# Kernel tuning notes

Measured on AMD Instinct MI355X. Metric: run time of the kernel, lower is better.

The kernel has to match this reference:

```python
import jax, jax.numpy as jnp
import numpy as np

EPS = 1e-12  # matches torch F.normalize clamp_min eps
SCALE = 20.0
NEG = -1e9


def l2norm(x):
    return x / jnp.maximum(jnp.linalg.norm(x, axis=-1, keepdims=True), EPS)


def setup_inputs() -> dict:
    key = jax.random.key(0)
    B, P, A, DV, DT, E = 32, 192, 30, 768, 768, 256
    ks = jax.random.split(key, 8)
    visual_feature = jax.random.normal(ks[0], (B, 1 + P, DV), jnp.float32)
    textual_feature = jax.random.normal(ks[1], (B, 1 + A, DT), jnp.float32)
    att_nums = jax.random.randint(ks[2], (B,), 1, A + 1)  # valid attr counts >=1
    # mask==1 marks padded attribute slots (consistent with att_nums)
    mask = (jnp.arange(A)[None, :] >= att_nums[:, None]).astype(jnp.int32)
    W_vis = 0.02 * jax.random.normal(ks[3], (E, DV), jnp.float32)
    W_txt = 0.02 * jax.random.normal(ks[4], (E, DT), jnp.float32)
    W_patch = 0.02 * jax.random.normal(ks[5], (E, DV), jnp.float32)
    W_att = 0.02 * jax.random.normal(ks[6], (E, DT), jnp.float32)
    z = jnp.zeros((E,), jnp.float32)
    return {
        "visual_feature": visual_feature, "textual_feature": textual_feature,
        "mask": mask, "att_nums": att_nums,
        "W_vis": W_vis, "b_vis": z, "W_txt": W_txt, "b_txt": z,
        "W_patch": W_patch, "b_patch": z, "W_att": W_att, "b_att": z,
    }


def reference(visual_feature, textual_feature, mask, att_nums,
              W_vis, b_vis, W_txt, b_txt, W_patch, b_patch, W_att, b_att):
    # token splits + linear projections
    visual_embed = visual_feature[:, 0] @ W_vis.T + b_vis        # [Bv, E]
    patch = visual_feature[:, 1:] @ W_patch.T + b_patch           # [Bv, P, E]
    textual_embed = textual_feature[:, 0] @ W_txt.T + b_txt       # [Bt, E]
    att = textual_feature[:, 1:] @ W_att.T + b_att                # [Bt, A, E]

    pad = mask.astype(bool)                                       # [Bt, A], True = padded

    # attention 1: each text's attributes attend over every image's patches
    s1 = jax.nn.relu(jnp.einsum('tae,vpe->vtap', l2norm(att), l2norm(patch))) * SCALE
    attn1 = jax.nn.softmax(s1, axis=-1)                           # [Bv, Bt, A, P]
    attend_patch = jnp.einsum('vtap,vpe->vtae', attn1, patch)     # [Bv, Bt, A, E]
    attend_patch = jnp.where(pad[None, :, :, None], 0.0, attend_patch)

    # attention 2: each image's patches attend over every text's attributes (masked)
    s2 = jax.nn.relu(jnp.einsum('vpe,tae->tvpa', l2norm(patch), l2norm(att))) * SCALE
    s2 = jnp.where(pad[:, None, None, :], NEG, s2)                # [Bt, Bv, P, A]
    attn2 = jax.nn.softmax(s2, axis=-1)
    attend_att = jnp.einsum('tvpa,tae->tvpe', attn2, att)         # [Bt, Bv, P, E]

    # local similarity
    ap = l2norm(attend_patch)                                     # [Bv, Bt, A, E]
    aa = l2norm(attend_att)                                       # [Bt, Bv, P, E]
    an = att_nums.astype(aa.dtype)
    sim = jnp.einsum('tvpe,vtae->tvpa', aa, ap) / an[:, None, None, None]
    local_similarity = sim.sum(axis=2).mean(axis=2)               # [Bt, Bv]

    # training-path global embeds
    patch_mean = patch.mean(axis=1)                               # [Bv, E]
    att_mean = (att / an[:, None, None]).sum(axis=1)              # [Bt, E]

    return (visual_embed, textual_embed, patch_mean, att_mean, local_similarity)
```

## Files before the change

### kernel.cpp

```cpp
#include <hip/hip_runtime.h>
#include <math.h>

#define D_IN 768
#define E_DIM 256
#define NB 32
#define NP 192
#define NA 30

#define A_SLOTS (452 * 24 * 64)
#define B_SLOTS (4 * 16 * 24 * 64)

typedef __attribute__((ext_vector_type(8))) __bf16 bf16x8;
typedef __attribute__((ext_vector_type(4))) float f32x4;

__device__ __forceinline__ bf16x8 cvt8(float4 a, float4 b) {
    bf16x8 v;
    v[0]=(__bf16)a.x; v[1]=(__bf16)a.y; v[2]=(__bf16)a.z; v[3]=(__bf16)a.w;
    v[4]=(__bf16)b.x; v[5]=(__bf16)b.y; v[6]=(__bf16)b.z; v[7]=(__bf16)b.w;
    return v;
}

__global__ __launch_bounds__(256) void prepack_kernel(
    const float* __restrict__ vf, const float* __restrict__ tf,
    const float* __restrict__ Wp, const float* __restrict__ Wa,
    const float* __restrict__ Wv, const float* __restrict__ Wt,
    __bf16* __restrict__ Apack, __bf16* __restrict__ Bpack,
    float* __restrict__ out_zero)
{
    const int s = blockIdx.x * 256 + threadIdx.x;
    if (s < 16384) out_zero[s] = 0.f;
    if (s < A_SLOTS) {
        const int r16 = s / 1536;
        const int rem = s - r16 * 1536;
        const int kt = rem >> 6, l = rem & 63;
        const int row16 = l & 15;
        const int k0 = kt * 32 + (l >> 4) * 8;
        const float* src;
        if (r16 < 384) {
            const int v = r16 / 12, sub = r16 - 12 * v;
            src = vf + (size_t)(v * 193 + 1 + sub * 16 + row16) * D_IN;
        } else if (r16 < 448) {
            const int u = r16 - 384, t = u >> 1, half = u & 1;
            const int ridx = half * 16 + row16;
            const int r = (ridx < NA) ? ridx : 0;
            src = tf + (size_t)(t * 31 + 1 + r) * D_IN;
        } else if (r16 < 450) {
            src = vf + (size_t)((r16 - 448) * 16 + row16) * 193 * D_IN;
        } else {
            src = tf + (size_t)((r16 - 450) * 16 + row16) * 31 * D_IN;
        }
        float4 f0 = *(const float4*)&src[k0];
        float4 f1 = *(const float4*)&src[k0 + 4];
        *(bf16x8*)&Apack[(size_t)s * 8] = cvt8(f0, f1);
    } else {
        const int u = s - A_SLOTS;
        const int mat = u / 24576;
        const int rem = u - mat * 24576;
        const int ntile = rem / 1536;
        const int rem2 = rem - ntile * 1536;
        const int kt = rem2 >> 6, l = rem2 & 63;
        const float* W;
        if (mat == 0)      W = Wp;
        else if (mat == 1) W = Wa;
        else if (mat == 2) W = Wv;
        else               W = Wt;
        const int k0 = kt * 32 + (l >> 4) * 8;
        const float* src = W + (size_t)(ntile * 16 + (l & 15)) * D_IN;
        float4 f0 = *(const float4*)&src[k0];
        float4 f1 = *(const float4*)&src[k0 + 4];
        *(bf16x8*)&Bpack[(size_t)u * 8] = cvt8(f0, f1);
    }
}

__global__ __launch_bounds__(256) void gemm_pack_kernel(
    const __bf16* __restrict__ Apack, const __bf16* __restrict__ Bpack,
    const float* __restrict__ bv, const float* __restrict__ bt,
    const float* __restrict__ bp, const float* __restrict__ ba,
    const int* __restrict__ att_nums,
    float* __restrict__ out_vis, float* __restrict__ out_txt,
    float* __restrict__ out_pm, float* __restrict__ out_am,
    __bf16* __restrict__ pn_frag, __bf16* __restrict__ pB_frag,
    __bf16* __restrict__ an_frag, __bf16* __restrict__ attT_frag)
{
    __shared__ float LDSf[16 * 260];
    __shared__ float invn_s[16];

    const int r16 = blockIdx.x;
    const int tid = threadIdx.x;
    const int w = tid >> 6, l = tid & 63, q = l >> 4, n15 = l & 15;
    const int mat = (r16 < 384) ? 0 : (r16 < 448) ? 1 : (r16 < 450) ? 2 : 3;
    const float* bias = (mat == 0) ? bp : (mat == 1) ? ba : (mat == 2) ? bv : bt;

    const __bf16* Ab = Apack + (size_t)r16 * 24 * 512 + l * 8;
    const __bf16* Bb = Bpack + ((size_t)(mat * 16 + w * 4) * 24 * 512) + l * 8;

    f32x4 acc[4];
    #pragma unroll
    for (int n = 0; n < 4; ++n) { f32x4 z = {0.f,0.f,0.f,0.f}; acc[n] = z; }

    #pragma unroll 6
    for (int kt = 0; kt < 24; ++kt) {
        bf16x8 a = *(const bf16x8*)&Ab[kt * 512];
        #pragma unroll
        for (int nt = 0; nt < 4; ++nt) {
            bf16x8 b = *(const bf16x8*)&Bb[(size_t)nt * 24 * 512 + kt * 512];
            acc[nt] = __builtin_amdgcn_mfma_f32_16x16x32_bf16(a, b, acc[nt], 0, 0, 0);
        }
    }

    #pragma unroll
    for (int nt = 0; nt < 4; ++nt) {
        const int col = w * 64 + nt * 16 + n15;
        const float b = bias[col];
        #pragma unroll
        for (int r = 0; r < 4; ++r)
            LDSf[(q * 4 + r) * 260 + col] = acc[nt][r] + b;
    }
    __syncthreads();

    if (mat >= 2) {
        float* outp = (mat == 2) ? out_vis : out_txt;
        const int rowbase = (mat == 2) ? (r16 - 448) * 16 : (r16 - 450) * 16;
        #pragma unroll
        for (int i = 0; i < 16; ++i)
            outp[(rowbase + i) * E_DIM + tid] = LDSf[i * 260 + tid];
        return;
    }

    const bool is_patch = (mat == 0);
    int vc = 0, mt = 0, t = 0, Av = 1;
    if (is_patch) {
        const int v = r16 / 12, sub = r16 - 12 * v;
        vc = v * 6 + (sub >> 1);  mt = sub & 1;
    } else {
        const int u = r16 - 384;
        t = u >> 1;  mt = u & 1;  Av = att_nums[t];
    }

    {
        const int row = tid >> 4, seg = tid & 15;
        const float* rr = &LDSf[row * 260 + seg * 16];
        float ssq = 0.f;
        #pragma unroll
        for (int j = 0; j < 16; ++j) ssq += rr[j] * rr[j];
        ssq += __shfl_xor(ssq, 1, 64);
        ssq += __shfl_xor(ssq, 2, 64);
        ssq += __shfl_xor(ssq, 4, 64);
        ssq += __shfl_xor(ssq, 8, 64);
        if (seg == 0) {
            const bool valid = is_patch || (mt * 16 + row < NA);
            invn_s[row] = valid ? 1.f / fmaxf(sqrtf(ssq), 1e-12f) : 0.f;
        }
    }
    {
        const int nrows = is_patch ? 16 : (mt == 0 ? 16 : 14);
        float s = 0.f;
        for (int r = 0; r < nrows; ++r) s += LDSf[r * 260 + tid];
        if (is_patch) atomicAdd(&out_pm[(r16 / 12) * E_DIM + tid], s * (1.f / 192.f));
        else          atomicAdd(&out_am[t * E_DIM + tid], s / (float)Av);
    }
    __syncthreads();

    {
        __bf16* dstn = (is_patch ? pn_frag + (size_t)vc * 8192
                                 : an_frag + (size_t)t * 8192) + (size_t)mt * 4096;
        #pragma unroll
        for (int ii = 0; ii < 2; ++ii) {
            const int s2 = tid + 256 * ii;
            const int koct = s2 >> 6, lane = s2 & 63;
            const int rloc = lane & 15;
            const int e0 = koct * 32 + (lane >> 4) * 8;
            const float inr = invn_s[rloc];
            const float* src = &LDSf[rloc * 260 + e0];
            bf16x8 vv;
            #pragma unroll
            for (int j = 0; j < 8; ++j) vv[j] = (__bf16)(src[j] * inr);
            *(bf16x8*)&dstn[(size_t)s2 * 8] = vv;
        }
    }
    {
        __bf16* dstb = is_patch ? pB_frag + (size_t)vc * 8192
                                : attT_frag + (size_t)t * 8192;
        #pragma unroll
        for (int ii = 0; ii < 2; ++ii) {
            const int s2 = tid + 256 * ii;
            const int nt = s2 >> 5, li = s2 & 31;
            const int lane = 32 * mt + li;
            const int p0 = (li >> 4) * 8;
            const int e = nt * 16 + (li & 15);
            bf16x8 vv;
            #pragma unroll
            for (int j = 0; j < 8; ++j) {
                float val = LDSf[(p0 + j) * 260 + e];
                if (!is_patch && (mt * 16 + p0 + j >= NA)) val = 0.f;
                vv[j] = (__bf16)val;
            }
            *(bf16x8*)&dstb[(size_t)(nt * 64 + lane) * 8] = vv;
        }
    }
}

__global__ __launch_bounds__(256, 3) void pair_mfma_kernel(
    const __bf16* __restrict__ pn_frag, const __bf16* __restrict__ pB_frag,
    const __bf16* __restrict__ an_frag, const __bf16* __restrict__ attT_frag,
    const int* __restrict__ att_nums, float* __restrict__ out_sim)
{
    __shared__ __align__(16) __bf16 an_s[8192];
    __shared__ __align__(16) __bf16 Xa_s[1024];
    __shared__ __align__(16) __bf16 XaT_s[1024];
    __shared__ float red_s[128];
    __shared__ float wred_s[4];

    const int v = blockIdx.x, t = blockIdx.y;
    const int tid = threadIdx.x;
    const int w = tid >> 6, l = tid & 63, q = l >> 4, n15 = l & 15;
    const int Av = att_nums[t];
    const int mt = w >> 1, at = w & 1;

    {
        const __bf16* s1 = an_frag + (size_t)t * 8192;
        #pragma unroll
        for (int i = 0; i < 4; ++i) {
            const int slot = tid + 256 * i;
            *(bf16x8*)&an_s[slot * 8] = *(const bf16x8*)&s1[slot * 8];
        }
    }
    __syncthreads();

    const __bf16* atb = attT_frag + (size_t)t * 8192;

    f32x4 apacc[2][4];
    #pragma unroll
    for (int m = 0; m < 2; ++m)
        #pragma unroll
        for (int n = 0; n < 4; ++n) { f32x4 z = {0.f,0.f,0.f,0.f}; apacc[m][n] = z; }
    float sa_acc[4] = {0.f, 0.f, 0.f, 0.f};

    for (int c = 0; c < 6; ++c) {
        const __bf16* pnb = pn_frag + (size_t)(v * 6 + c) * 8192;
        const __bf16* pbb = pB_frag + (size_t)(v * 6 + c) * 8192;

        bf16x8 pb[4], ab[4];
        #pragma unroll
        for (int n = 0; n < 4; ++n) {
            pb[n] = *(const bf16x8*)&pbb[((w * 4 + n) * 64 + l) * 8];
            ab[n] = *(const bf16x8*)&atb[((w * 4 + n) * 64 + l) * 8];
        }

        {
            f32x4 sacc = {0.f, 0.f, 0.f, 0.f};
            #pragma unroll
            for (int kp = 0; kp < 8; ++kp) {
                bf16x8 af  = *(const bf16x8*)&pnb[((mt * 8 + kp) * 64 + l) * 8];
                bf16x8 bf_ = *(const bf16x8*)&an_s[((at * 8 + kp) * 64 + l) * 8];
                sacc = __builtin_amdgcn_mfma_f32_16x16x32_bf16(af, bf_, sacc, 0, 0, 0);
            }
            const int a = at * 16 + n15;
            #pragma unroll
            for (int r = 0; r < 4; ++r) {
                const int pcl = q * 4 + r;
                const int pcc = mt * 16 + pcl;
                float xvv = (a < Av) ? __expf(fmaxf(20.f * sacc[r], 0.f)) : 0.f;
                __bf16 h = (__bf16)xvv;
                Xa_s[mt * 512 + (pcl + 16 * (a >> 3)) * 8 + (a & 7)] = h;
                XaT_s[at * 512 + (n15 + 16 * (pcc >> 3)) * 8 + (pcc & 7)] = h;
            }
        }
        __syncthreads();

        f32x4 aacc[2][4];
        {
            bf16x8 xa0 = *(const bf16x8*)&Xa_s[l * 8];
            bf16x8 xa1 = *(const bf16x8*)&Xa_s[512 + l * 8];
            bf16x8 xt0 = *(const bf16x8*)&XaT_s[l * 8];
            bf16x8 xt1 = *(const bf16x8*)&XaT_s[512 + l * 8];
            #pragma unroll
            for (int n = 0; n < 4; ++n) {
                f32x4 z = {0.f, 0.f, 0.f, 0.f};
                aacc[0][n] = __builtin_amdgcn_mfma_f32_16x16x32_bf16(xa0, ab[n], z, 0, 0, 0);
                aacc[1][n] = __builtin_amdgcn_mfma_f32_16x16x32_bf16(xa1, ab[n], z, 0, 0, 0);
                apacc[0][n] = __builtin_amdgcn_mfma_f32_16x16x32_bf16(xt0, pb[n], apacc[0][n], 0, 0, 0);
                apacc[1][n] = __builtin_amdgcn_mfma_f32_16x16x32_bf16(xt1, pb[n], apacc[1][n], 0, 0, 0);
            }
        }
        #pragma unroll
        for (int mt2 = 0; mt2 < 2; ++mt2)
            #pragma unroll
            for (int r = 0; r < 4; ++r) {
                float ssq = 0.f;
                #pragma unroll
                for (int n = 0; n < 4; ++n) { float vv = aacc[mt2][n][r]; ssq += vv * vv; }
                ssq += __shfl_xor(ssq, 1, 64);
                ssq += __shfl_xor(ssq, 2, 64);
                ssq += __shfl_xor(ssq, 4, 64);
                ssq += __shfl_xor(ssq, 8, 64);
                if (n15 == 0) red_s[(mt2 * 16 + q * 4 + r) * 4 + w] = ssq;
            }
        __syncthreads();
        #pragma unroll
        for (int mt2 = 0; mt2 < 2; ++mt2)
            #pragma unroll
            for (int r = 0; r < 4; ++r) {
                const int row = mt2 * 16 + q * 4 + r;
                const float s = red_s[row * 4] + red_s[row * 4 + 1]
                              + red_s[row * 4 + 2] + red_s[row * 4 + 3];
                const float inr = 1.f / fmaxf(sqrtf(s), 1e-12f);
                #pragma unroll
                for (int n = 0; n < 4; ++n) sa_acc[n] += aacc[mt2][n][r] * inr;
            }
    }

    __syncthreads();
    #pragma unroll
    for (int mt2 = 0; mt2 < 2; ++mt2)
        #pragma unroll
        for (int r = 0; r < 4; ++r) {
            float ssq = 0.f;
            #pragma unroll
            for (int n = 0; n < 4; ++n) { float vv = apacc[mt2][n][r]; ssq += vv * vv; }
            ssq += __shfl_xor(ssq, 1, 64);
            ssq += __shfl_xor(ssq, 2, 64);
            ssq += __shfl_xor(ssq, 4, 64);
            ssq += __shfl_xor(ssq, 8, 64);
            if (n15 == 0) red_s[(mt2 * 16 + q * 4 + r) * 4 + w] = ssq;
        }
    __syncthreads();

    float inr_ap[2][4];
    #pragma unroll
    for (int mt2 = 0; mt2 < 2; ++mt2)
        #pragma unroll
        for (int r = 0; r < 4; ++r) {
            const int row = mt2 * 16 + q * 4 + r;
            const float s = red_s[row * 4] + red_s[row * 4 + 1]
                          + red_s[row * 4 + 2] + red_s[row * 4 + 3];
            inr_ap[mt2][r] = 1.f / fmaxf(sqrtf(s), 1e-12f);
        }

    float prod = 0.f;
    #pragma unroll
    for (int n = 0; n < 4; ++n) {
        float sp = 0.f;
        #pragma unroll
        for (int mt2 = 0; mt2 < 2; ++mt2)
            #pragma unroll
            for (int r = 0; r < 4; ++r)
                sp += apacc[mt2][n][r] * inr_ap[mt2][r];
        float saf = sa_acc[n];
        saf += __shfl_xor(saf, 16, 64);
        saf += __shfl_xor(saf, 32, 64);
        float spf = sp;
        spf += __shfl_xor(spf, 16, 64);
        spf += __shfl_xor(spf, 32, 64);
        prod += saf * spf;
    }
    prod += __shfl_xor(prod, 1, 64);
    prod += __shfl_xor(prod, 2, 64);
    prod += __shfl_xor(prod, 4, 64);
    prod += __shfl_xor(prod, 8, 64);
    prod += __shfl_xor(prod, 16, 64);
    prod += __shfl_xor(prod, 32, 64);
    if (l == 0) wred_s[w] = prod;
    __syncthreads();
    if (tid == 0)
        out_sim[t * NB + v] = (wred_s[0] + wred_s[1] + wred_s[2] + wred_s[3]) * 0.25f
                              / ((float)Av * 30.f);
}

extern "C" void kernel_launch(void* const* d_in, const int* in_sizes, int n_in,
                              void* d_out, int out_size, void* d_ws, size_t ws_size,
                              hipStream_t stream)
{
    const float* vf = (const float*)d_in[0];
    const float* tf = (const float*)d_in[1];
    const int*   an = (const int*)d_in[3];
    const float* Wv = (const float*)d_in[4];
    const float* bv = (const float*)d_in[5];
    const float* Wt = (const float*)d_in[6];
    const float* bt = (const float*)d_in[7];
    const float* Wp = (const float*)d_in[8];
    const float* bp = (const float*)d_in[9];
    const float* Wa = (const float*)d_in[10];
    const float* ba = (const float*)d_in[11];

    float* out = (float*)d_out;
    float* out_vis = out;
    float* out_txt = out + 8192;
    float* out_pm  = out + 16384;
    float* out_am  = out + 24576;
    float* out_sim = out + 32768;

    __bf16* Apack = (__bf16*)d_ws;
    __bf16* Bpack = Apack + (size_t)A_SLOTS * 8;
    __bf16* frag0 = Bpack + (size_t)B_SLOTS * 8;
    __bf16* pn_frag   = frag0;
    __bf16* pB_frag   = frag0 + 1572864;
    __bf16* an_frag   = frag0 + 3145728;
    __bf16* attT_frag = frag0 + 3407872;

    prepack_kernel<<<(A_SLOTS + B_SLOTS) / 256, 256, 0, stream>>>(
        vf, tf, Wp, Wa, Wv, Wt, Apack, Bpack, out + 16384);

    gemm_pack_kernel<<<452, 256, 0, stream>>>(
        Apack, Bpack, bv, bt, bp, ba, an,
        out_vis, out_txt, out_pm, out_am,
        pn_frag, pB_frag, an_frag, attT_frag);

    pair_mfma_kernel<<<dim3(NB, NB), 256, 0, stream>>>(
        pn_frag, pB_frag, an_frag, attT_frag, an, out_sim);
}
```

Before: 149.6 us.

## Split GEMM K across 8 waves and restructure pair kernel to process chunk pairs

The projection GEMM kernel now runs 512 threads per block and splits the K dimension across two halves of waves, combining the partial sums through an extra LDS buffer. The pair kernel now processes two patch chunks per iteration. Each wave computes full-width attribute rows, so the attended-attribute norm is reduced in registers instead of through an LDS round trip, and there are half as many barriers. The cost is higher register pressure (16 accumulator tiles per wave) and an extra LDS reduction stage in the GEMM.

Result: slower. 178.4 us (+19.2%).

```diff
diff --git a/kernel.cpp b/kernel.cpp
--- a/kernel.cpp
+++ b/kernel.cpp
@@ -72,7 +72,7 @@
     }
 }
 
-__global__ __launch_bounds__(256) void gemm_pack_kernel(
+__global__ __launch_bounds__(512) void gemm_pack_kernel(
     const __bf16* __restrict__ Apack, const __bf16* __restrict__ Bpack,
     const float* __restrict__ bv, const float* __restrict__ bt,
     const float* __restrict__ bp, const float* __restrict__ ba,
@@ -83,23 +83,26 @@
     __bf16* __restrict__ an_frag, __bf16* __restrict__ attT_frag)
 {
     __shared__ float LDSf[16 * 260];
+    __shared__ float LDSp[16 * 260];
     __shared__ float invn_s[16];
 
     const int r16 = blockIdx.x;
     const int tid = threadIdx.x;
     const int w = tid >> 6, l = tid & 63, q = l >> 4, n15 = l & 15;
+    const int kh = w >> 2, wq = w & 3;
     const int mat = (r16 < 384) ? 0 : (r16 < 448) ? 1 : (r16 < 450) ? 2 : 3;
     const float* bias = (mat == 0) ? bp : (mat == 1) ? ba : (mat == 2) ? bv : bt;
 
-    const __bf16* Ab = Apack + (size_t)r16 * 24 * 512 + l * 8;
-    const __bf16* Bb = Bpack + ((size_t)(mat * 16 + w * 4) * 24 * 512) + l * 8;
+    const __bf16* Ab = Apack + (size_t)r16 * 24 * 512 + (size_t)kh * 12 * 512 + l * 8;
+    const __bf16* Bb = Bpack + ((size_t)(mat * 16 + wq * 4) * 24 * 512)
+                             + (size_t)kh * 12 * 512 + l * 8;
 
     f32x4 acc[4];
     #pragma unroll
     for (int n = 0; n < 4; ++n) { f32x4 z = {0.f,0.f,0.f,0.f}; acc[n] = z; }
 
     #pragma unroll 6
-    for (int kt = 0; kt < 24; ++kt) {
+    for (int kt = 0; kt < 12; ++kt) {
         bf16x8 a = *(const bf16x8*)&Ab[kt * 512];
         #pragma unroll
         for (int nt = 0; nt < 4; ++nt) {
@@ -108,22 +111,37 @@
         }
     }
 
-    #pragma unroll
-    for (int nt = 0; nt < 4; ++nt) {
-        const int col = w * 64 + nt * 16 + n15;
-        const float b = bias[col];
-        #pragma unroll
-        for (int r = 0; r < 4; ++r)
-            LDSf[(q * 4 + r) * 260 + col] = acc[nt][r] + b;
+    if (kh == 1) {
+        #pragma unroll
+        for (int nt = 0; nt < 4; ++nt) {
+            const int col = wq * 64 + nt * 16 + n15;
+            #pragma unroll
+            for (int r = 0; r < 4; ++r)
+                LDSp[(q * 4 + r) * 260 + col] = acc[nt][r];
+        }
+    }
+    __syncthreads();
+    if (kh == 0) {
+        #pragma unroll
+        for (int nt = 0; nt < 4; ++nt) {
+            const int col = wq * 64 + nt * 16 + n15;
+            const float b = bias[col];
+            #pragma unroll
+            for (int r = 0; r < 4; ++r) {
+                const int row = q * 4 + r;
+                LDSf[row * 260 + col] = acc[nt][r] + LDSp[row * 260 + col] + b;
+            }
+        }
     }
     __syncthreads();
 
     if (mat >= 2) {
         float* outp = (mat == 2) ? out_vis : out_txt;
         const int rowbase = (mat == 2) ? (r16 - 448) * 16 : (r16 - 450) * 16;
-        #pragma unroll
-        for (int i = 0; i < 16; ++i)
-            outp[(rowbase + i) * E_DIM + tid] = LDSf[i * 260 + tid];
+        const int col = tid & 255, rh = tid >> 8;
+        #pragma unroll
+        for (int i = 0; i < 8; ++i)
+            outp[(rowbase + rh * 8 + i) * E_DIM + col] = LDSf[(rh * 8 + i) * 260 + col];
         return;
     }
 
@@ -138,21 +156,22 @@
     }
 
     {
-        const int row = tid >> 4, seg = tid & 15;
-        const float* rr = &LDSf[row * 260 + seg * 16];
+        const int row = tid >> 5, seg = tid & 31;
+        const float* rr = &LDSf[row * 260 + seg * 8];
         float ssq = 0.f;
         #pragma unroll
-        for (int j = 0; j < 16; ++j) ssq += rr[j] * rr[j];
+        for (int j = 0; j < 8; ++j) ssq += rr[j] * rr[j];
         ssq += __shfl_xor(ssq, 1, 64);
         ssq += __shfl_xor(ssq, 2, 64);
         ssq += __shfl_xor(ssq, 4, 64);
         ssq += __shfl_xor(ssq, 8, 64);
+        ssq += __shfl_xor(ssq, 16, 64);
         if (seg == 0) {
             const bool valid = is_patch || (mt * 16 + row < NA);
             invn_s[row] = valid ? 1.f / fmaxf(sqrtf(ssq), 1e-12f) : 0.f;
         }
     }
-    {
+    if (tid < 256) {
         const int nrows = is_patch ? 16 : (mt == 0 ? 16 : 14);
         float s = 0.f;
         for (int r = 0; r < nrows; ++r) s += LDSf[r * 260 + tid];
@@ -164,39 +183,33 @@
     {
         __bf16* dstn = (is_patch ? pn_frag + (size_t)vc * 8192
                                  : an_frag + (size_t)t * 8192) + (size_t)mt * 4096;
-        #pragma unroll
-        for (int ii = 0; ii < 2; ++ii) {
-            const int s2 = tid + 256 * ii;
-            const int koct = s2 >> 6, lane = s2 & 63;
-            const int rloc = lane & 15;
-            const int e0 = koct * 32 + (lane >> 4) * 8;
-            const float inr = invn_s[rloc];
-            const float* src = &LDSf[rloc * 260 + e0];
-            bf16x8 vv;
-            #pragma unroll
-            for (int j = 0; j < 8; ++j) vv[j] = (__bf16)(src[j] * inr);
-            *(bf16x8*)&dstn[(size_t)s2 * 8] = vv;
-        }
+        const int s2 = tid;
+        const int koct = s2 >> 6, lane = s2 & 63;
+        const int rloc = lane & 15;
+        const int e0 = koct * 32 + (lane >> 4) * 8;
+        const float inr = invn_s[rloc];
+        const float* src = &LDSf[rloc * 260 + e0];
+        bf16x8 vv;
+        #pragma unroll
+        for (int j = 0; j < 8; ++j) vv[j] = (__bf16)(src[j] * inr);
+        *(bf16x8*)&dstn[(size_t)s2 * 8] = vv;
     }
     {
         __bf16* dstb = is_patch ? pB_frag + (size_t)vc * 8192
                                 : attT_frag + (size_t)t * 8192;
-        #pragma unroll
-        for (int ii = 0; ii < 2; ++ii) {
-            const int s2 = tid + 256 * ii;
-            const int nt = s2 >> 5, li = s2 & 31;
-            const int lane = 32 * mt + li;
-            const int p0 = (li >> 4) * 8;
-            const int e = nt * 16 + (li & 15);
-            bf16x8 vv;
-            #pragma unroll
-            for (int j = 0; j < 8; ++j) {
-                float val = LDSf[(p0 + j) * 260 + e];
-                if (!is_patch && (mt * 16 + p0 + j >= NA)) val = 0.f;
-                vv[j] = (__bf16)val;
-            }
-            *(bf16x8*)&dstb[(size_t)(nt * 64 + lane) * 8] = vv;
-        }
+        const int s2 = tid;
+        const int nt = s2 >> 5, li = s2 & 31;
+        const int lane = 32 * mt + li;
+        const int p0 = (li >> 4) * 8;
+        const int e = nt * 16 + (li & 15);
+        bf16x8 vv;
+        #pragma unroll
+        for (int j = 0; j < 8; ++j) {
+            float val = LDSf[(p0 + j) * 260 + e];
+            if (!is_patch && (mt * 16 + p0 + j >= NA)) val = 0.f;
+            vv[j] = (__bf16)val;
+        }
+        *(bf16x8*)&dstb[(size_t)(nt * 64 + lane) * 8] = vv;
     }
 }
 
@@ -206,9 +219,10 @@
     const int* __restrict__ att_nums, float* __restrict__ out_sim)
 {
     __shared__ __align__(16) __bf16 an_s[8192];
-    __shared__ __align__(16) __bf16 Xa_s[1024];
-    __shared__ __align__(16) __bf16 XaT_s[1024];
+    __shared__ __align__(16) __bf16 Xa_s[2][1024];
+    __shared__ __align__(16) __bf16 XaT_s[2][1024];
     __shared__ float red_s[128];
+    __shared__ float sp_s[256];
     __shared__ float wred_s[4];
 
     const int v = blockIdx.x, t = blockIdx.y;
@@ -216,6 +230,7 @@
     const int w = tid >> 6, l = tid & 63, q = l >> 4, n15 = l & 15;
     const int Av = att_nums[t];
     const int mt = w >> 1, at = w & 1;
+    const int cp = w >> 1, mtx = w & 1;
 
     {
         const __bf16* s1 = an_frag + (size_t)t * 8192;
@@ -234,20 +249,14 @@
     for (int m = 0; m < 2; ++m)
         #pragma unroll
         for (int n = 0; n < 4; ++n) { f32x4 z = {0.f,0.f,0.f,0.f}; apacc[m][n] = z; }
-    float sa_acc[4] = {0.f, 0.f, 0.f, 0.f};
-
-    for (int c = 0; c < 6; ++c) {
-        const __bf16* pnb = pn_frag + (size_t)(v * 6 + c) * 8192;
-        const __bf16* pbb = pB_frag + (size_t)(v * 6 + c) * 8192;
-
-        bf16x8 pb[4], ab[4];
-        #pragma unroll
-        for (int n = 0; n < 4; ++n) {
-            pb[n] = *(const bf16x8*)&pbb[((w * 4 + n) * 64 + l) * 8];
-            ab[n] = *(const bf16x8*)&atb[((w * 4 + n) * 64 + l) * 8];
-        }
-
-        {
+    float sa_acc[16];
+    #pragma unroll
+    for (int n = 0; n < 16; ++n) sa_acc[n] = 0.f;
+
+    for (int i = 0; i < 3; ++i) {
+        #pragma unroll
+        for (int cc = 0; cc < 2; ++cc) {
+            const __bf16* pnb = pn_frag + (size_t)(v * 6 + 2 * i + cc) * 8192;
             f32x4 sacc = {0.f, 0.f, 0.f, 0.f};
             #pragma unroll
             for (int kp = 0; kp < 8; ++kp) {
@@ -262,108 +271,106 @@
                 const int pcc = mt * 16 + pcl;
                 float xvv = (a < Av) ? __expf(fmaxf(20.f * sacc[r], 0.f)) : 0.f;
                 __bf16 h = (__bf16)xvv;
-                Xa_s[mt * 512 + (pcl + 16 * (a >> 3)) * 8 + (a & 7)] = h;
-                XaT_s[at * 512 + (n15 + 16 * (pcc >> 3)) * 8 + (pcc & 7)] = h;
+                Xa_s[cc][mt * 512 + (pcl + 16 * (a >> 3)) * 8 + (a & 7)] = h;
+                XaT_s[cc][at * 512 + (n15 + 16 * (pcc >> 3)) * 8 + (pcc & 7)] = h;
             }
         }
         __syncthreads();
 
-        f32x4 aacc[2][4];
         {
-            bf16x8 xa0 = *(const bf16x8*)&Xa_s[l * 8];
-            bf16x8 xa1 = *(const bf16x8*)&Xa_s[512 + l * 8];
-            bf16x8 xt0 = *(const bf16x8*)&XaT_s[l * 8];
-            bf16x8 xt1 = *(const bf16x8*)&XaT_s[512 + l * 8];
-            #pragma unroll
-            for (int n = 0; n < 4; ++n) {
+            bf16x8 xa = *(const bf16x8*)&Xa_s[cp][mtx * 512 + l * 8];
+            f32x4 aacc[16];
+            #pragma unroll
+            for (int nt = 0; nt < 16; ++nt) {
+                bf16x8 ab = *(const bf16x8*)&atb[(nt * 64 + l) * 8];
                 f32x4 z = {0.f, 0.f, 0.f, 0.f};
-                aacc[0][n] = __builtin_amdgcn_mfma_f32_16x16x32_bf16(xa0, ab[n], z, 0, 0, 0);
-                aacc[1][n] = __builtin_amdgcn_mfma_f32_16x16x32_bf16(xa1, ab[n], z, 0, 0, 0);
-                apacc[0][n] = __builtin_amdgcn_mfma_f32_16x16x32_bf16(xt0, pb[n], apacc[0][n], 0, 0, 0);
-                apacc[1][n] = __builtin_amdgcn_mfma_f32_16x16x32_bf16(xt1, pb[n], apacc[1][n], 0, 0, 0);
-            }
-        }
-        #pragma unroll
-        for (int mt2 = 0; mt2 < 2; ++mt2)
+                aacc[nt] = __builtin_amdgcn_mfma_f32_16x16x32_bf16(xa, ab, z, 0, 0, 0);
+            }
             #pragma unroll
             for (int r = 0; r < 4; ++r) {
                 float ssq = 0.f;
                 #pragma unroll
-                for (int n = 0; n < 4; ++n) { float vv = aacc[mt2][n][r]; ssq += vv * vv; }
+                for (int nt = 0; nt < 16; ++nt) ssq += aacc[nt][r] * aacc[nt][r];
                 ssq += __shfl_xor(ssq, 1, 64);
                 ssq += __shfl_xor(ssq, 2, 64);
                 ssq += __shfl_xor(ssq, 4, 64);
                 ssq += __shfl_xor(ssq, 8, 64);
-                if (n15 == 0) red_s[(mt2 * 16 + q * 4 + r) * 4 + w] = ssq;
-            }
+                const float inr = 1.f / fmaxf(sqrtf(ssq), 1e-12f);
+                #pragma unroll
+                for (int nt = 0; nt < 16; ++nt) sa_acc[nt] += aacc[nt][r] * inr;
+            }
+        }
+        #pragma unroll
+        for (int cp2 = 0; cp2 < 2; ++cp2) {
+            const __bf16* pbb = pB_frag + (size_t)(v * 6 + 2 * i + cp2) * 8192;
+            bf16x8 xt0 = *(const bf16x8*)&XaT_s[cp2][l * 8];
+            bf16x8 xt1 = *(const bf16x8*)&XaT_s[cp2][512 + l * 8];
+            #pragma unroll
+            for (int nt = 0; nt < 4; ++nt) {
+                bf16x8 pbv = *(const bf16x8*)&pbb[((w * 4 + nt) * 64 + l) * 8];
+                apacc[0][nt] = __builtin_amdgcn_mfma_f32_16x16x32_bf16(xt0, pbv, apacc[0][nt], 0, 0, 0);
+                apacc[1][nt] = __builtin_amdgcn_mfma_f32_16x16x32_bf16(xt1, pbv, apacc[1][nt], 0, 0, 0);
+            }
+        }
         __syncthreads();
-        #pragma unroll
-        for (int mt2 = 0; mt2 < 2; ++mt2)
-            #pragma unroll
-            for (int r = 0; r < 4; ++r) {
-                const int row = mt2 * 16 + q * 4 + r;
-                const float s = red_s[row * 4] + red_s[row * 4 + 1]
-                              + red_s[row * 4 + 2] + red_s[row * 4 + 3];
-                const float inr = 1.f / fmaxf(sqrtf(s), 1e-12f);
-                #pragma unroll
-                for (int n = 0; n < 4; ++n) sa_acc[n] += aacc[mt2][n][r] * inr;
-            }
-    }
-
-    __syncthreads();
-    #pragma unroll
-    for (int mt2 = 0; mt2 < 2; ++mt2)
+    }
+
+    #pragma unroll
+    for (int atx = 0; atx < 2; ++atx)
         #pragma unroll
         for (int r = 0; r < 4; ++r) {
             float ssq = 0.f;
             #pragma unroll
-            for (int n = 0; n < 4; ++n) { float vv = apacc[mt2][n][r]; ssq += vv * vv; }
+            for (int nt = 0; nt < 4; ++nt) { float vv = apacc[atx][nt][r]; ssq += vv * vv; }
             ssq += __shfl_xor(ssq, 1, 64);
             ssq += __shfl_xor(ssq, 2, 64);
             ssq += __shfl_xor(ssq, 4, 64);
             ssq += __shfl_xor(ssq, 8, 64);
-            if (n15 == 0) red_s[(mt2 * 16 + q * 4 + r) * 4 + w] = ssq;
-        }
-    __syncthreads();
-
+            if (n15 == 0) red_s[(atx * 16 + q * 4 + r) * 4 + w] = ssq;
+        }
+    __syncthreads();
     float inr_ap[2][4];
     #pragma unroll
-    for (int mt2 = 0; mt2 < 2; ++mt2)
+    for (int atx = 0; atx < 2; ++atx)
         #pragma unroll
         for (int r = 0; r < 4; ++r) {
-            const int row = mt2 * 16 + q * 4 + r;
+            const int row = atx * 16 + q * 4 + r;
             const float s = red_s[row * 4] + red_s[row * 4 + 1]
                           + red_s[row * 4 + 2] + red_s[row * 4 + 3];
-            inr_ap[mt2][r] = 1.f / fmaxf(sqrtf(s), 1e-12f);
-        }
+            inr_ap[atx][r] = 1.f / fmaxf(sqrtf(s), 1e-12f);
+        }
+
+    #pragma unroll
+    for (int nt = 0; nt < 4; ++nt) {
+        float sp = 0.f;
+        #pragma unroll
+        for (int atx = 0; atx < 2; ++atx)
+            #pragma unroll
+            for (int r = 0; r < 4; ++r)
+                sp += apacc[atx][nt][r] * inr_ap[atx][r];
+        sp += __shfl_xor(sp, 16, 64);
+        sp += __shfl_xor(sp, 32, 64);
+        if (q == 0) sp_s[(w * 4 + nt) * 16 + n15] = sp;
+    }
+    #pragma unroll
+    for (int nt = 0; nt < 16; ++nt) {
+        sa_acc[nt] += __shfl_xor(sa_acc[nt], 16, 64);
+        sa_acc[nt] += __shfl_xor(sa_acc[nt], 32, 64);
+    }
+    __syncthreads();
 
     float prod = 0.f;
     #pragma unroll
-    for (int n = 0; n < 4; ++n) {
-        float sp = 0.f;
-        #pragma unroll
-        for (int mt2 = 0; mt2 < 2; ++mt2)
-            #pragma unroll
-            for (int r = 0; r < 4; ++r)
-                sp += apacc[mt2][n][r] * inr_ap[mt2][r];
-        float saf = sa_acc[n];
-        saf += __shfl_xor(saf, 16, 64);
-        saf += __shfl_xor(saf, 32, 64);
-        float spf = sp;
-        spf += __shfl_xor(spf, 16, 64);
-        spf += __shfl_xor(spf, 32, 64);
-        prod += saf * spf;
-    }
+    for (int nt = 0; nt < 16; ++nt)
+        prod += sa_acc[nt] * sp_s[nt * 16 + n15];
     prod += __shfl_xor(prod, 1, 64);
     prod += __shfl_xor(prod, 2, 64);
     prod += __shfl_xor(prod, 4, 64);
     prod += __shfl_xor(prod, 8, 64);
-    prod += __shfl_xor(prod, 16, 64);
-    prod += __shfl_xor(prod, 32, 64);
     if (l == 0) wred_s[w] = prod;
     __syncthreads();
     if (tid == 0)
-        out_sim[t * NB + v] = (wred_s[0] + wred_s[1] + wred_s[2] + wred_s[3]) * 0.25f
+        out_sim[t * NB + v] = (wred_s[0] + wred_s[1] + wred_s[2] + wred_s[3])
                               / ((float)Av * 30.f);
 }
 
@@ -401,7 +408,7 @@
     prepack_kernel<<<(A_SLOTS + B_SLOTS) / 256, 256, 0, stream>>>(
         vf, tf, Wp, Wa, Wv, Wt, Apack, Bpack, out + 16384);
 
-    gemm_pack_kernel<<<452, 256, 0, stream>>>(
+    gemm_pack_kernel<<<452, 512, 0, stream>>>(
         Apack, Bpack, bv, bt, bp, ba, an,
         out_vis, out_txt, out_pm, out_am,
         pn_frag, pB_frag, an_frag, attT_frag);
```
